# Kernel optimization log

Hardware: AMD Instinct MI355X
Metric: run time of the kernel (lower is better)

The kernel has to match this reference:

```python
import jax, jax.numpy as jnp
import numpy as np

MATCH_IOU = 0.5
IGNORE_IOU = 0.4
BOX_VARIANCE = jnp.asarray([0.1, 0.1, 0.2, 0.2], dtype=jnp.float32)
BACKGROUND_CLASS = -1.0
IGNORE_CLASS = -2.0

M_ANCHORS = 76725  # RetinaNet P3-P7 on 640x640, 9 anchors/loc
BATCH = 16
N_GT = 100
NUM_CLASSES = 20


def setup_inputs() -> dict:
    key = jax.random.key(0)
    k1, k2, k3, k4, k5 = jax.random.split(key, 5)
    # anchors in xywh (top-left x, y, width, height)
    axy = jax.random.uniform(k1, (M_ANCHORS, 2), minval=0.0, maxval=600.0)
    awh = jax.random.uniform(k2, (M_ANCHORS, 2), minval=16.0, maxval=256.0)
    anchor_boxes = jnp.concatenate([axy, awh], axis=-1).astype(jnp.float32)
    # gt boxes [B, N, 5] = [x, y, w, h, class_id] in xywh
    gxy = jax.random.uniform(k3, (BATCH, N_GT, 2), minval=0.0, maxval=600.0)
    gwh = jax.random.uniform(k4, (BATCH, N_GT, 2), minval=8.0, maxval=200.0)
    gcls = jax.random.randint(k5, (BATCH, N_GT, 1), 0, NUM_CLASSES).astype(jnp.float32)
    gt_boxes = jnp.concatenate([gxy, gwh, gcls], axis=-1)
    return {"anchor_boxes": anchor_boxes, "gt_boxes": gt_boxes}


def _xywh_to_corners(b):
    x, y, w, h = b[..., 0], b[..., 1], b[..., 2], b[..., 3]
    return x, y, x + w, y + h


def _pairwise_iou(anchors, gt):
    # anchors: [M, 4], gt: [B, N, 4] -> iou: [B, M, N]
    ax1, ay1, ax2, ay2 = _xywh_to_corners(anchors)          # [M]
    gx1, gy1, gx2, gy2 = _xywh_to_corners(gt)               # [B, N]
    ax1 = ax1[None, :, None]; ay1 = ay1[None, :, None]
    ax2 = ax2[None, :, None]; ay2 = ay2[None, :, None]
    gx1 = gx1[:, None, :]; gy1 = gy1[:, None, :]
    gx2 = gx2[:, None, :]; gy2 = gy2[:, None, :]
    iw = jnp.maximum(jnp.minimum(ax2, gx2) - jnp.maximum(ax1, gx1), 0.0)
    ih = jnp.maximum(jnp.minimum(ay2, gy2) - jnp.maximum(ay1, gy1), 0.0)
    inter = iw * ih                                          # [B, M, N]
    a_area = (anchors[:, 2] * anchors[:, 3])[None, :, None]
    g_area = (gt[..., 2] * gt[..., 3])[:, None, :]
    union = a_area + g_area - inter
    return jnp.where(union > 0.0, inter / union, 0.0)


def reference(anchor_boxes, gt_boxes):
    # anchor_boxes: [M, 4] xywh; gt_boxes: [B, N, 5] xywh + class
    gt_xywh = gt_boxes[..., :4]
    cls_ids = gt_boxes[..., 4]                               # [B, N]

    iou = _pairwise_iou(anchor_boxes, gt_xywh)               # [B, M, N]
    max_iou = jnp.max(iou, axis=-1)                          # [B, M]
    matched_gt_idx = jnp.argmax(iou, axis=-1)                # [B, M]
    positive_mask = max_iou >= MATCH_IOU
    negative_mask = max_iou < IGNORE_IOU
    ignore_mask = jnp.logical_not(positive_mask | negative_mask)

    # gather matched gt boxes / classes: [B, M, 5]
    matched = jnp.take_along_axis(gt_boxes, matched_gt_idx[..., None], axis=1)
    mx, my, mw, mh = matched[..., 0], matched[..., 1], matched[..., 2], matched[..., 3]
    matched_cls = matched[..., 4]

    # encode xywh -> center deltas, scaled by variance
    acx = anchor_boxes[:, 0] + 0.5 * anchor_boxes[:, 2]
    acy = anchor_boxes[:, 1] + 0.5 * anchor_boxes[:, 3]
    aw = anchor_boxes[:, 2]
    ah = anchor_boxes[:, 3]
    gcx = mx + 0.5 * mw
    gcy = my + 0.5 * mh
    box_target = jnp.stack(
        [
            (gcx - acx[None, :]) / aw[None, :],
            (gcy - acy[None, :]) / ah[None, :],
            jnp.log(mw / aw[None, :]),
            jnp.log(mh / ah[None, :]),
        ],
        axis=-1,
    ) / BOX_VARIANCE                                          # [B, M, 4]

    cls_target = jnp.where(positive_mask, matched_cls, BACKGROUND_CLASS)
    cls_target = jnp.where(ignore_mask, IGNORE_CLASS, cls_target)

    label = jnp.concatenate([box_target, cls_target[..., None]], axis=-1)  # [B, M, 5]
    any_nan = jnp.any(jnp.isnan(label), axis=-1, keepdims=True)
    label = jnp.where(any_nan, IGNORE_CLASS, label)
    return label
```

## Files before the change

### kernel.cpp

```cpp
#include <hip/hip_runtime.h>
#include <math.h>

#define M_ANCHORS 76725
#define BATCH     16
#define N_GT      100
#define MATCH_IOU  0.5f
#define IGNORE_IOU 0.4f

__global__ __launch_bounds__(256) void retina_encode_kernel(
    const float* __restrict__ anchors,
    const float* __restrict__ gt,
    float* __restrict__ out)
{
#pragma clang fp contract(off)
    __shared__ float4 s_box[N_GT];
    __shared__ float  s_ga[N_GT];
    __shared__ float  s_raw[N_GT * 5];

    const int b = blockIdx.y;
    const int a = blockIdx.x * blockDim.x + threadIdx.x;

    for (int i = threadIdx.x; i < N_GT * 5; i += blockDim.x)
        s_raw[i] = gt[b * (N_GT * 5) + i];
    __syncthreads();
    if (threadIdx.x < N_GT) {
        const int j = threadIdx.x;
        const float gx = s_raw[j * 5 + 0];
        const float gy = s_raw[j * 5 + 1];
        const float gw = s_raw[j * 5 + 2];
        const float gh = s_raw[j * 5 + 3];
        s_box[j] = make_float4(gx, gy, gx + gw, gy + gh);
        s_ga[j]  = gw * gh;
    }
    __syncthreads();

    if (a >= M_ANCHORS) return;

    const float4 av = *reinterpret_cast<const float4*>(anchors + (size_t)a * 4);
    const float ax1 = av.x, ay1 = av.y, aw = av.z, ah = av.w;
    const float ax2 = ax1 + aw;
    const float ay2 = ay1 + ah;
    const float aarea = aw * ah;

    float bestInter = 0.0f;
    float bestS     = 1.0f;
    int   bidx      = 0;
    int   flagged   = 0;

    #pragma unroll 10
    for (int j = 0; j < N_GT; ++j) {
        const float4 g = s_box[j];
        float iw = fminf(ax2, g.z) - fmaxf(ax1, g.x);
        iw = fmaxf(iw, 0.0f);
        float ih = fminf(ay2, g.w) - fmaxf(ay1, g.y);
        ih = fmaxf(ih, 0.0f);
        const float inter = iw * ih;
        const float S  = aarea + s_ga[j];
        const float pj = inter * bestS;
        const float pb = bestInter * S;
        const float d  = pj - pb;
        const float tol = fmaf(4e-6f, pb, -1e-33f);
        flagged |= (fabsf(d) <= tol);
        if (d > 0.0f) { bestInter = inter; bestS = S; bidx = j; }
    }

    float M;
    if (!flagged) {
        M = bestInter / (bestS - bestInter);
    } else {
        float best = -1.0f;
        bidx = 0;
        for (int j = 0; j < N_GT; ++j) {
            const float4 g = s_box[j];
            float iw = fminf(ax2, g.z) - fmaxf(ax1, g.x);
            iw = fmaxf(iw, 0.0f);
            float ih = fminf(ay2, g.w) - fmaxf(ay1, g.y);
            ih = fmaxf(ih, 0.0f);
            const float inter = iw * ih;
            const float uni = (aarea + s_ga[j]) - inter;
            const float iou = (uni > 0.0f) ? (inter / uni) : 0.0f;
            if (iou > best) { best = iou; bidx = j; }
        }
        M = best;
    }

    const float mx   = s_raw[bidx * 5 + 0];
    const float my   = s_raw[bidx * 5 + 1];
    const float mw   = s_raw[bidx * 5 + 2];
    const float mh   = s_raw[bidx * 5 + 3];
    const float mcls = s_raw[bidx * 5 + 4];

    const float acx = ax1 + 0.5f * aw;
    const float acy = ay1 + 0.5f * ah;
    const float gcx = mx + 0.5f * mw;
    const float gcy = my + 0.5f * mh;

    float t0 = ((gcx - acx) / aw) / 0.1f;
    float t1 = ((gcy - acy) / ah) / 0.1f;
    float t2 = logf(mw / aw) / 0.2f;
    float t3 = logf(mh / ah) / 0.2f;

    const bool pos = (M >= MATCH_IOU);
    const bool neg = (M < IGNORE_IOU);
    float cls = pos ? mcls : -1.0f;
    if (!pos && !neg) cls = -2.0f;

    if (isnan(t0) || isnan(t1) || isnan(t2) || isnan(t3) || isnan(cls)) {
        t0 = t1 = t2 = t3 = cls = -2.0f;
    }

    float* o = out + ((size_t)b * M_ANCHORS + a) * 5;
    o[0] = t0;
    o[1] = t1;
    o[2] = t2;
    o[3] = t3;
    o[4] = cls;
}

extern "C" void kernel_launch(void* const* d_in, const int* in_sizes, int n_in,
                              void* d_out, int out_size, void* d_ws, size_t ws_size,
                              hipStream_t stream) {
    const float* anchors = (const float*)d_in[0];
    const float* gt      = (const float*)d_in[1];
    float* out           = (float*)d_out;

    const dim3 block(256, 1, 1);
    const dim3 grid((M_ANCHORS + 255) / 256, BATCH, 1);
    retina_encode_kernel<<<grid, block, 0, stream>>>(anchors, gt, out);
}
```

Baseline: 79.16 us.

## Split GT matching loop across two threads per anchor with shuffle merge

Each anchor is now handled by a pair of lanes, each scanning half of the ground-truth boxes. The two partial best matches and tie flags are merged with cross-lane shuffles. The grid doubles to keep one anchor per lane pair. This shortens the serial per-thread loop and adds more waves for latency hiding, and the inner loop drops one clamp and fuses one multiply-subtract. In exchange, half the lanes sit idle during the encode and store epilogue, and the stores are less dense.

```diff
diff --git a/kernel.cpp b/kernel.cpp
--- a/kernel.cpp
+++ b/kernel.cpp
@@ -4,6 +4,7 @@
 #define M_ANCHORS 76725
 #define BATCH     16
 #define N_GT      100
+#define HALF_GT   50
 #define MATCH_IOU  0.5f
 #define IGNORE_IOU 0.4f
 
@@ -18,19 +19,20 @@
     __shared__ float  s_raw[N_GT * 5];
 
     const int b = blockIdx.y;
-    const int a = blockIdx.x * blockDim.x + threadIdx.x;
+    const int t = threadIdx.x;
+    const int a = blockIdx.x * 128 + (t >> 1);
+    const int half = t & 1;
 
-    for (int i = threadIdx.x; i < N_GT * 5; i += blockDim.x)
+    for (int i = t; i < N_GT * 5; i += blockDim.x)
         s_raw[i] = gt[b * (N_GT * 5) + i];
     __syncthreads();
-    if (threadIdx.x < N_GT) {
-        const int j = threadIdx.x;
-        const float gx = s_raw[j * 5 + 0];
-        const float gy = s_raw[j * 5 + 1];
-        const float gw = s_raw[j * 5 + 2];
-        const float gh = s_raw[j * 5 + 3];
-        s_box[j] = make_float4(gx, gy, gx + gw, gy + gh);
-        s_ga[j]  = gw * gh;
+    if (t < N_GT) {
+        const float gx = s_raw[t * 5 + 0];
+        const float gy = s_raw[t * 5 + 1];
+        const float gw = s_raw[t * 5 + 2];
+        const float gh = s_raw[t * 5 + 3];
+        s_box[t] = make_float4(gx, gy, gx + gw, gy + gh);
+        s_ga[t]  = gw * gh;
     }
     __syncthreads();
 
@@ -42,40 +44,56 @@
     const float ay2 = ay1 + ah;
     const float aarea = aw * ah;
 
-    float bestInter = 0.0f;
-    float bestS     = 1.0f;
-    int   bidx      = 0;
-    int   flagged   = 0;
+    const int jbase = half ? HALF_GT : 0;
+
+    float bI = 0.0f;
+    float bS = 1.0f;
+    int   bj = jbase;
+    bool  flag = false;
 
     #pragma unroll 10
-    for (int j = 0; j < N_GT; ++j) {
+    for (int jj = 0; jj < HALF_GT; ++jj) {
+        const int j = jbase + jj;
         const float4 g = s_box[j];
-        float iw = fminf(ax2, g.z) - fmaxf(ax1, g.x);
-        iw = fmaxf(iw, 0.0f);
+        float iw = fmaxf(fminf(ax2, g.z) - fmaxf(ax1, g.x), 0.0f);
         float ih = fminf(ay2, g.w) - fmaxf(ay1, g.y);
-        ih = fmaxf(ih, 0.0f);
         const float inter = iw * ih;
-        const float S  = aarea + s_ga[j];
-        const float pj = inter * bestS;
-        const float pb = bestInter * S;
-        const float d  = pj - pb;
+        const float S   = aarea + s_ga[j];
+        const float pb  = bI * S;
+        const float d   = fmaf(inter, bS, -pb);
         const float tol = fmaf(4e-6f, pb, -1e-33f);
-        flagged |= (fabsf(d) <= tol);
-        if (d > 0.0f) { bestInter = inter; bestS = S; bidx = j; }
+        flag = flag | (fabsf(d) <= tol);
+        if (d > 0.0f) { bI = inter; bS = S; bj = j; }
     }
 
+    const float oI = __shfl_xor(bI, 1);
+    const float oS = __shfl_xor(bS, 1);
+    const int   oj = __shfl_xor(bj, 1);
+    const int   of = __shfl_xor((int)flag, 1);
+
+    if (half) return;
+
+    bool anyflag = flag | (of != 0);
+    const float pA = oI * bS;
+    const float pB = bI * oS;
+    const float dd = pA - pB;
+    const float ptol = fmaf(4e-6f, fmaxf(pA, pB), -1e-33f);
+    anyflag = anyflag | (fabsf(dd) <= ptol);
+
+    float BI = bI, BS = bS;
+    int   bidx = bj;
+    if (dd > 0.0f) { BI = oI; BS = oS; bidx = oj; }
+
     float M;
-    if (!flagged) {
-        M = bestInter / (bestS - bestInter);
+    if (!anyflag) {
+        M = BI / (BS - BI);
     } else {
         float best = -1.0f;
         bidx = 0;
         for (int j = 0; j < N_GT; ++j) {
             const float4 g = s_box[j];
-            float iw = fminf(ax2, g.z) - fmaxf(ax1, g.x);
-            iw = fmaxf(iw, 0.0f);
-            float ih = fminf(ay2, g.w) - fmaxf(ay1, g.y);
-            ih = fmaxf(ih, 0.0f);
+            float iw = fmaxf(fminf(ax2, g.z) - fmaxf(ax1, g.x), 0.0f);
+            float ih = fmaxf(fminf(ay2, g.w) - fmaxf(ay1, g.y), 0.0f);
             const float inter = iw * ih;
             const float uni = (aarea + s_ga[j]) - inter;
             const float iou = (uni > 0.0f) ? (inter / uni) : 0.0f;
@@ -125,6 +143,6 @@
     float* out           = (float*)d_out;
 
     const dim3 block(256, 1, 1);
-    const dim3 grid((M_ANCHORS + 255) / 256, BATCH, 1);
+    const dim3 grid((M_ANCHORS + 127) / 128, BATCH, 1);
     retina_encode_kernel<<<grid, block, 0, stream>>>(anchors, gt, out);
 }
```

Result: faster. 76.58 us (-3.3%).
